# Optimization experiments

Hardware: AMD Instinct MI355X
Metric: run time of the kernel (lower is better)

The kernel has to match this reference:

```python
import jax, jax.numpy as jnp
import numpy as np
import math

SLIDING_WINDOW = 1024  # matches init kwarg

def setup_inputs() -> dict:
    key = jax.random.key(0)
    ks = jax.random.split(key, 6)
    B, S, Hq, Hkv, D = 1, 2048, 32, 8, 128
    NUM_PAGES, STRIDE = 300, 16
    q = jax.random.normal(ks[0], (B, S, Hq, D), dtype=jnp.float32)
    k = jax.random.normal(ks[1], (B, S, Hkv, D), dtype=jnp.float32)
    v = jax.random.normal(ks[2], (B, S, Hkv, D), dtype=jnp.float32)
    sink = jax.random.normal(ks[3], (Hq,), dtype=jnp.float32)
    cache_state = jnp.zeros((NUM_PAGES, STRIDE, 2, Hkv, D), dtype=jnp.float32)
    seq_block_ids = jax.random.randint(ks[4], (B, S // STRIDE), 0, NUM_PAGES, dtype=jnp.int64)
    return {"q": q, "k": k, "v": v, "sink": sink,
            "cache_state": cache_state, "seq_block_ids": seq_block_ids}


def reference(q, k, v, sink, cache_state, seq_block_ids):
    B, S, Hq, D = q.shape
    Hkv = k.shape[2]
    stride = cache_state.shape[1]

    # --- paged cache write (prefill side effect) ---
    kv = jnp.stack([k, v], axis=2)                       # [B,S,2,Hkv,D]
    pages = kv.reshape(B * (S // stride), stride, 2, Hkv, D)
    _ = cache_state.at[seq_block_ids.reshape(-1)].set(pages)

    # --- decomposed attention: matmul + mask + softmax(+sink) + matmul ---
    rep = Hq // Hkv
    ke = jnp.repeat(k, rep, axis=2)                      # [B,S,Hq,D] (GQA expand)
    ve = jnp.repeat(v, rep, axis=2)
    scale = 1.0 / math.sqrt(D)
    scores = jnp.einsum('bihd,bjhd->bhij', q, ke) * scale  # [B,Hq,S,S]

    i = jnp.arange(S)[:, None]
    j = jnp.arange(S)[None, :]
    allowed = (j <= i) & (i - j < SLIDING_WINDOW)        # causal + sliding window
    neg = jnp.finfo(scores.dtype).min
    logits = jnp.where(allowed, scores, neg)

    # attention sink: extra per-head logit appended; contributes to denominator only
    sink_l = jnp.broadcast_to(sink[None, :, None, None], (B, Hq, S, 1))
    probs = jax.nn.softmax(jnp.concatenate([logits, sink_l], axis=-1), axis=-1)[..., :S]

    out = jnp.einsum('bhij,bjhd->bihd', probs, ve)       # [B,S,Hq,D]
    return out
```

## Files before the change

### kernel.cpp

```cpp
#include <hip/hip_runtime.h>
#include <hip/hip_bf16.h>


#define S_LEN 2048
#define DH    128
#define HQ    32
#define HKV   8
#define WIN   1024
#define BR    64
#define BC    32
#define NT    (S_LEN / BC)
#define FM    16.0f
#define TILE_CH 512

typedef unsigned short u16;
typedef __attribute__((ext_vector_type(8))) short  short8;
typedef __attribute__((ext_vector_type(4))) float  floatx4;
typedef __attribute__((ext_vector_type(4))) unsigned int uintx4;

__device__ __forceinline__ unsigned rne1(float a) {
    unsigned u = __float_as_uint(a);
    return (u + 0x7FFFu + ((u >> 16) & 1u)) >> 16;
}
__device__ __forceinline__ unsigned rne_pk(float a, float b) {
    return rne1(a) | (rne1(b) << 16);
}

__global__ __launch_bounds__(256) void pack_kv(const float* __restrict__ kg,
                                               const float* __restrict__ vg,
                                               u16* __restrict__ kp,
                                               u16* __restrict__ vtp)
{
    __shared__ float Vs[BC][DH + 1];
    const int b   = blockIdx.x;
    const int hk  = b >> 6;
    const int jt  = b & 63;
    const int tid = threadIdx.x;
    const int j0  = jt * BC;

    #pragma unroll
    for (int t = 0; t < 4; t++) {
        int idx = tid + t * 256;
        int j   = idx >> 5;
        int dc  = idx & 31;
        floatx4 f = *(const floatx4*)(vg + ((size_t)(j0 + j) * HKV + hk) * DH + dc * 4);
        Vs[j][dc * 4 + 0] = f[0]; Vs[j][dc * 4 + 1] = f[1];
        Vs[j][dc * 4 + 2] = f[2]; Vs[j][dc * 4 + 3] = f[3];
    }

    u16* kpt = kp + (size_t)b * TILE_CH * 8;
    #pragma unroll
    for (int t = 0; t < 2; t++) {
        int c = tid + t * 256;
        int row = c >> 4, cc = c & 15;
        const float* p = kg + ((size_t)(j0 + row) * HKV + hk) * DH + cc * 8;
        floatx4 f0 = *(const floatx4*)p;
        floatx4 f1 = *(const floatx4*)(p + 4);
        int pc = (row << 4) | (cc ^ (row & 7));
        *(uintx4*)(kpt + pc * 8) =
            (uintx4){rne_pk(f0[0], f0[1]), rne_pk(f0[2], f0[3]),
                     rne_pk(f1[0], f1[1]), rne_pk(f1[2], f1[3])};
    }
    __syncthreads();

    u16* vpt = vtp + (size_t)b * TILE_CH * 8;
    #pragma unroll
    for (int t = 0; t < 2; t++) {
        int q  = tid + t * 256;
        int dd = q >> 2, c = q & 3;
        unsigned w0 = rne_pk(Vs[c * 4 + 0][dd], Vs[c * 4 + 16][dd]);
        unsigned w1 = rne_pk(Vs[c * 4 + 1][dd], Vs[c * 4 + 17][dd]);
        unsigned w2 = rne_pk(Vs[c * 4 + 2][dd], Vs[c * 4 + 18][dd]);
        unsigned w3 = rne_pk(Vs[c * 4 + 3][dd], Vs[c * 4 + 19][dd]);
        int qp = (dd << 2) | (c ^ ((dd >> 2) & 3));
        *(uintx4*)(vpt + qp * 8) = (uintx4){w0, w1, w2, w3};
    }
}

__launch_bounds__(256, 4)
__global__ void fa_kernel(const float* __restrict__ qg,
                          const u16* __restrict__ kp,
                          const u16* __restrict__ vtp,
                          const float* __restrict__ sg,
                          float* __restrict__ outg)
{
    __shared__ __align__(16) u16 Kt[2][TILE_CH * 8];
    __shared__ __align__(16) u16 Vt[2][TILE_CH * 8];
    __shared__ __align__(16) u16 Pb[BR * 40];

    const int tid  = threadIdx.x;
    const int w    = tid >> 6;
    const int lane = tid & 63;
    const int quad = lane >> 4;
    const int l16  = lane & 15;

    const int bid  = blockIdx.x;
    const int hk   = bid & 7;
    const int idx  = bid >> 3;
    const int hrem = idx & 3;
    const int u5   = (idx >> 2) & 7;
    const int t4   = idx >> 5;
    const int qbt[4] = {u5, 15 - u5, 16 + u5, 31 - u5};
    const int qb   = qbt[t4];
    const int h    = hk * 4 + hrem;

    const int i0 = qb * BR;
    const int m0 = i0 + w * 16;

    short8 qf[4];
    {
        const float* qrow = qg + ((size_t)(m0 + l16) * HQ + h) * DH;
        #pragma unroll
        for (int kk = 0; kk < 4; kk++) {
            const float* p = qrow + kk * 32 + quad * 8;
            floatx4 f0 = *(const floatx4*)p;
            floatx4 f1 = *(const floatx4*)(p + 4);
            uintx4 u = (uintx4){rne_pk(f0[0], f0[1]), rne_pk(f0[2], f0[3]),
                                rne_pk(f1[0], f1[1]), rne_pk(f1[2], f1[3])};
            qf[kk] = *(short8*)&u;
        }
    }

    floatx4 acc[8];
    #pragma unroll
    for (int i = 0; i < 8; i++) acc[i] = (floatx4){0.f, 0.f, 0.f, 0.f};
    float l_part[4] = {0.f, 0.f, 0.f, 0.f};

    int c_r[4];
    #pragma unroll
    for (int r = 0; r < 4; r++) c_r[r] = m0 + quad * 4 + r - l16;

    int jlo = i0 - (WIN - 1); if (jlo < 0) jlo = 0;
    const int jt_lo = jlo >> 5;
    const int jt_hi = (i0 + BR - 1) >> 5;

    const float SC2 = 0.08838834764831845f * 1.4426950408889634f;

    const int ch0 = w * 64 + lane;
    auto stage = [&](int bb, int jt) {
        const u16* kpt = kp  + ((size_t)(hk * NT + jt)) * TILE_CH * 8;
        const u16* vpt = vtp + ((size_t)(hk * NT + jt)) * TILE_CH * 8;
        #pragma unroll
        for (int it = 0; it < 2; it++) {
            int ch = ch0 + it * 256;
            __builtin_amdgcn_global_load_lds(
                (const __attribute__((address_space(1))) unsigned*)(kpt + ch * 8),
                (__attribute__((address_space(3))) unsigned*)(&Kt[bb][ch * 8]), 16, 0, 0);
            __builtin_amdgcn_global_load_lds(
                (const __attribute__((address_space(1))) unsigned*)(vpt + ch * 8),
                (__attribute__((address_space(3))) unsigned*)(&Vt[bb][ch * 8]), 16, 0, 0);
        }
    };

    stage(0, jt_lo);
    int bb = 0;

    for (int jt = jt_lo; jt <= jt_hi; jt++) {
        const int j0 = jt << 5;

        __syncthreads();

        if (jt < jt_hi) stage(bb ^ 1, jt + 1);

        floatx4 sc[2];
        sc[0] = (floatx4){0.f, 0.f, 0.f, 0.f};
        sc[1] = (floatx4){0.f, 0.f, 0.f, 0.f};
        #pragma unroll
        for (int kk = 0; kk < 4; kk++) {
            #pragma unroll
            for (int n = 0; n < 2; n++) {
                int row = n * 16 + l16;
                int cc  = kk * 4 + quad;
                int pc  = (row << 4) | (cc ^ (row & 7));
                short8 kf = *(const short8*)(&Kt[bb][pc * 8]);
                sc[n] = __builtin_amdgcn_mfma_f32_16x16x32_bf16(qf[kk], kf, sc[n], 0, 0, 0);
            }
        }

        const int prow0 = w * 16 + quad * 4;
        const bool interior = (j0 + (BC - 1) <= i0) && (j0 >= i0 + BR - WIN);
        if (interior) {
            #pragma unroll
            for (int r = 0; r < 4; r++) {
                float p0 = exp2f(fmaf(sc[0][r], SC2, -FM));
                float p1 = exp2f(fmaf(sc[1][r], SC2, -FM));
                l_part[r] += p0 + p1;
                *(unsigned*)(&Pb[(prow0 + r) * 40 + l16 * 2]) = rne_pk(p0, p1);
            }
        } else {
            #pragma unroll
            for (int r = 0; r < 4; r++) {
                bool a0 = (j0 <= c_r[r]) && (j0 > c_r[r] - WIN);
                bool a1 = (j0 + 16 <= c_r[r]) && (j0 + 16 > c_r[r] - WIN);
                float p0 = a0 ? exp2f(fmaf(sc[0][r], SC2, -FM)) : 0.f;
                float p1 = a1 ? exp2f(fmaf(sc[1][r], SC2, -FM)) : 0.f;
                l_part[r] += p0 + p1;
                *(unsigned*)(&Pb[(prow0 + r) * 40 + l16 * 2]) = rne_pk(p0, p1);
            }
        }

        {
            short8 pf = *(const short8*)(&Pb[(w * 16 + l16) * 40 + quad * 8]);
            #pragma unroll
            for (int nf = 0; nf < 8; nf++) {
                int dd = nf * 16 + l16;
                int qp = (dd << 2) | (quad ^ ((dd >> 2) & 3));
                short8 vf = *(const short8*)(&Vt[bb][qp * 8]);
                acc[nf] = __builtin_amdgcn_mfma_f32_16x16x32_bf16(pf, vf, acc[nf], 0, 0, 0);
            }
        }
        bb ^= 1;
    }

    const float sk2 = exp2f(fmaf(sg[h], 1.4426950408889634f, -FM));
    float inv[4];
    #pragma unroll
    for (int r = 0; r < 4; r++) {
        float l = l_part[r];
        #pragma unroll
        for (int off = 1; off < 16; off <<= 1)
            l += __shfl_xor(l, off);
        inv[r] = 1.f / (l + sk2);
    }
    #pragma unroll
    for (int nf = 0; nf < 8; nf++) {
        int d = nf * 16 + l16;
        #pragma unroll
        for (int r = 0; r < 4; r++) {
            int ig = m0 + quad * 4 + r;
            outg[((size_t)ig * HQ + h) * DH + d] = acc[nf][r] * inv[r];
        }
    }
}

__launch_bounds__(256, 4)
__global__ void fa_fallback(const float* __restrict__ qg,
                            const float* __restrict__ kg,
                            const float* __restrict__ vg,
                            const float* __restrict__ sg,
                            float* __restrict__ outg)
{
    __shared__ __align__(16) u16 Kt[BC * DH];
    __shared__ __align__(16) u16 Vt[DH * BC];
    __shared__ __align__(16) u16 Pb[BR * 40];

    const int tid  = threadIdx.x;
    const int w    = tid >> 6;
    const int lane = tid & 63;
    const int quad = lane >> 4;
    const int l16  = lane & 15;

    const int qb = blockIdx.x / HQ;
    const int h  = blockIdx.x % HQ;
    const int hk = h >> 2;
    const int i0 = qb * BR;
    const int m0 = i0 + w * 16;

    short8 qf[4];
    {
        const float* qrow = qg + ((size_t)(m0 + l16) * HQ + h) * DH;
        #pragma unroll
        for (int kk = 0; kk < 4; kk++) {
            const float* p = qrow + kk * 32 + quad * 8;
            floatx4 f0 = *(const floatx4*)p;
            floatx4 f1 = *(const floatx4*)(p + 4);
            uintx4 u = (uintx4){rne_pk(f0[0], f0[1]), rne_pk(f0[2], f0[3]),
                                rne_pk(f1[0], f1[1]), rne_pk(f1[2], f1[3])};
            qf[kk] = *(short8*)&u;
        }
    }

    floatx4 acc[8];
    #pragma unroll
    for (int i = 0; i < 8; i++) acc[i] = (floatx4){0.f, 0.f, 0.f, 0.f};
    float l_part[4] = {0.f, 0.f, 0.f, 0.f};

    int jlo = i0 - (WIN - 1); if (jlo < 0) jlo = 0;
    const int jt_lo = jlo >> 5;
    const int jt_hi = (i0 + BR - 1) >> 5;
    const float SC2 = 0.08838834764831845f * 1.4426950408889634f;

    for (int jt = jt_lo; jt <= jt_hi; jt++) {
        const int j0 = jt << 5;
        __syncthreads();
        #pragma unroll
        for (int it = 0; it < 2; it++) {
            int g   = tid + 256 * it;
            int row = g >> 4, cc = g & 15;
            int pc  = (row << 4) | (cc ^ (row & 7));
            const float* kpp = kg + ((size_t)(j0 + row) * HKV + hk) * DH + cc * 8;
            floatx4 f0 = *(const floatx4*)kpp;
            floatx4 f1 = *(const floatx4*)(kpp + 4);
            *(uintx4*)(&Kt[pc * 8]) =
                (uintx4){rne_pk(f0[0], f0[1]), rne_pk(f0[2], f0[3]),
                         rne_pk(f1[0], f1[1]), rne_pk(f1[2], f1[3])};
        }
        #pragma unroll
        for (int it = 0; it < 2; it++) {
            int g  = tid + 256 * it;
            int d  = g & 127, jc = g >> 7;
            const float* vp = vg + ((size_t)(j0 + jc * 8) * HKV + hk) * DH + d;
            float e0 = vp[0 * HKV * DH], e1 = vp[1 * HKV * DH];
            float e2 = vp[2 * HKV * DH], e3 = vp[3 * HKV * DH];
            float e4 = vp[4 * HKV * DH], e5 = vp[5 * HKV * DH];
            float e6 = vp[6 * HKV * DH], e7 = vp[7 * HKV * DH];
            int pc = (d << 2) | (jc ^ ((d >> 2) & 3));
            *(uintx4*)(&Vt[pc * 8]) =
                (uintx4){rne_pk(e0, e1), rne_pk(e2, e3), rne_pk(e4, e5), rne_pk(e6, e7)};
        }
        __syncthreads();

        floatx4 sc[2];
        sc[0] = (floatx4){0.f, 0.f, 0.f, 0.f};
        sc[1] = (floatx4){0.f, 0.f, 0.f, 0.f};
        #pragma unroll
        for (int kk = 0; kk < 4; kk++) {
            #pragma unroll
            for (int n = 0; n < 2; n++) {
                int row = n * 16 + l16;
                int cc  = kk * 4 + quad;
                int pc  = (row << 4) | (cc ^ (row & 7));
                short8 kf = *(const short8*)(&Kt[pc * 8]);
                sc[n] = __builtin_amdgcn_mfma_f32_16x16x32_bf16(qf[kk], kf, sc[n], 0, 0, 0);
            }
        }
        #pragma unroll
        for (int r = 0; r < 4; r++) {
            int   i_g = m0 + quad * 4 + r;
            int   jg0 = j0 + l16, jg1 = j0 + 16 + l16;
            bool  a0  = (jg0 <= i_g) && (i_g - jg0 < WIN);
            bool  a1  = (jg1 <= i_g) && (i_g - jg1 < WIN);
            float p0  = a0 ? exp2f(fmaf(sc[0][r], SC2, -FM)) : 0.f;
            float p1  = a1 ? exp2f(fmaf(sc[1][r], SC2, -FM)) : 0.f;
            l_part[r] += p0 + p1;
            int prow = w * 16 + quad * 4 + r;
            *(unsigned*)(&Pb[prow * 40 + 2 * l16]) = rne_pk(p0, p1);
        }
        {
            short8 pf = *(const short8*)(&Pb[(w * 16 + l16) * 40 + quad * 8]);
            #pragma unroll
            for (int nf = 0; nf < 8; nf++) {
                int dd = nf * 16 + l16;
                int qp = (dd << 2) | (quad ^ ((dd >> 2) & 3));
                short8 vf = *(const short8*)(&Vt[qp * 8]);
                acc[nf] = __builtin_amdgcn_mfma_f32_16x16x32_bf16(pf, vf, acc[nf], 0, 0, 0);
            }
        }
    }

    const float sk2 = exp2f(fmaf(sg[h], 1.4426950408889634f, -FM));
    float inv[4];
    #pragma unroll
    for (int r = 0; r < 4; r++) {
        float l = l_part[r];
        #pragma unroll
        for (int off = 1; off < 16; off <<= 1)
            l += __shfl_xor(l, off);
        inv[r] = 1.f / (l + sk2);
    }
    #pragma unroll
    for (int nf = 0; nf < 8; nf++) {
        int d = nf * 16 + l16;
        #pragma unroll
        for (int r = 0; r < 4; r++) {
            int ig = m0 + quad * 4 + r;
            outg[((size_t)ig * HQ + h) * DH + d] = acc[nf][r] * inv[r];
        }
    }
}

extern "C" void kernel_launch(void* const* d_in, const int* in_sizes, int n_in,
                              void* d_out, int out_size, void* d_ws, size_t ws_size,
                              hipStream_t stream) {
    const float* q  = (const float*)d_in[0];
    const float* k  = (const float*)d_in[1];
    const float* v  = (const float*)d_in[2];
    const float* sk = (const float*)d_in[3];
    float* out = (float*)d_out;

    const size_t tile_elems = (size_t)HKV * NT * TILE_CH * 8;
    const size_t need = 2 * tile_elems * sizeof(u16);

    if (ws_size >= need) {
        u16* kp  = (u16*)d_ws;
        u16* vtp = kp + tile_elems;
        pack_kv<<<dim3(HKV * NT), 256, 0, stream>>>(k, v, kp, vtp);
        fa_kernel<<<dim3((S_LEN / BR) * HQ), 256, 0, stream>>>(q, kp, vtp, sk, out);
    } else {
        fa_fallback<<<dim3((S_LEN / BR) * HQ), 256, 0, stream>>>(q, k, v, sk, out);
    }
}
```

Baseline: 163.1 us.

## Keep P in registers via transposed QK MFMA, drop LDS P buffer

```diff
diff --git a/kernel.cpp b/kernel.cpp
--- a/kernel.cpp
+++ b/kernel.cpp
@@ -24,6 +24,11 @@
 }
 __device__ __forceinline__ unsigned rne_pk(float a, float b) {
     return rne1(a) | (rne1(b) << 16);
+}
+__device__ __forceinline__ unsigned cvt_pk(float a, float b) {
+    unsigned r;
+    asm("v_cvt_pk_bf16_f32 %0, %1, %2" : "=v"(r) : "v"(a), "v"(b));
+    return r;
 }
 
 __global__ __launch_bounds__(256) void pack_kv(const float* __restrict__ kg,
@@ -77,7 +82,7 @@
     }
 }
 
-__launch_bounds__(256, 4)
+__launch_bounds__(256, 5)
 __global__ void fa_kernel(const float* __restrict__ qg,
                           const u16* __restrict__ kp,
                           const u16* __restrict__ vtp,
@@ -86,7 +91,6 @@
 {
     __shared__ __align__(16) u16 Kt[2][TILE_CH * 8];
     __shared__ __align__(16) u16 Vt[2][TILE_CH * 8];
-    __shared__ __align__(16) u16 Pb[BR * 40];
 
     const int tid  = threadIdx.x;
     const int w    = tid >> 6;
@@ -115,20 +119,34 @@
             const float* p = qrow + kk * 32 + quad * 8;
             floatx4 f0 = *(const floatx4*)p;
             floatx4 f1 = *(const floatx4*)(p + 4);
-            uintx4 u = (uintx4){rne_pk(f0[0], f0[1]), rne_pk(f0[2], f0[3]),
-                                rne_pk(f1[0], f1[1]), rne_pk(f1[2], f1[3])};
-            qf[kk] = *(short8*)&u;
-        }
+            uintx4 uq = (uintx4){cvt_pk(f0[0], f0[1]), cvt_pk(f0[2], f0[3]),
+                                 cvt_pk(f1[0], f1[1]), cvt_pk(f1[2], f1[3])};
+            qf[kk] = *(short8*)&uq;
+        }
+    }
+
+    int kpc[8];
+    #pragma unroll
+    for (int n = 0; n < 2; n++) {
+        int row = n * 16 + l16;
+        #pragma unroll
+        for (int kk = 0; kk < 4; kk++)
+            kpc[n * 4 + kk] = (((row << 4) | ((kk * 4 + quad) ^ (row & 7)))) * 8;
+    }
+    int vqp[8];
+    #pragma unroll
+    for (int nf = 0; nf < 8; nf++) {
+        int dd = nf * 16 + l16;
+        vqp[nf] = ((dd << 2) | (quad ^ ((dd >> 2) & 3))) * 8;
     }
 
     floatx4 acc[8];
     #pragma unroll
     for (int i = 0; i < 8; i++) acc[i] = (floatx4){0.f, 0.f, 0.f, 0.f};
-    float l_part[4] = {0.f, 0.f, 0.f, 0.f};
-
-    int c_r[4];
-    #pragma unroll
-    for (int r = 0; r < 4; r++) c_r[r] = m0 + quad * 4 + r - l16;
+    float l_sum = 0.f;
+
+    const int ci  = m0 + l16;
+    const int qb4 = quad * 4;
 
     int jlo = i0 - (WIN - 1); if (jlo < 0) jlo = 0;
     const int jt_lo = jlo >> 5;
@@ -162,73 +180,67 @@
 
         if (jt < jt_hi) stage(bb ^ 1, jt + 1);
 
-        floatx4 sc[2];
-        sc[0] = (floatx4){0.f, 0.f, 0.f, 0.f};
-        sc[1] = (floatx4){0.f, 0.f, 0.f, 0.f};
+        floatx4 ss[2];
+        ss[0] = (floatx4){0.f, 0.f, 0.f, 0.f};
+        ss[1] = (floatx4){0.f, 0.f, 0.f, 0.f};
         #pragma unroll
         for (int kk = 0; kk < 4; kk++) {
-            #pragma unroll
-            for (int n = 0; n < 2; n++) {
-                int row = n * 16 + l16;
-                int cc  = kk * 4 + quad;
-                int pc  = (row << 4) | (cc ^ (row & 7));
-                short8 kf = *(const short8*)(&Kt[bb][pc * 8]);
-                sc[n] = __builtin_amdgcn_mfma_f32_16x16x32_bf16(qf[kk], kf, sc[n], 0, 0, 0);
-            }
-        }
-
-        const int prow0 = w * 16 + quad * 4;
+            short8 kf0 = *(const short8*)(&Kt[bb][kpc[kk]]);
+            short8 kf1 = *(const short8*)(&Kt[bb][kpc[4 + kk]]);
+            ss[0] = __builtin_amdgcn_mfma_f32_16x16x32_bf16(kf0, qf[kk], ss[0], 0, 0, 0);
+            ss[1] = __builtin_amdgcn_mfma_f32_16x16x32_bf16(kf1, qf[kk], ss[1], 0, 0, 0);
+        }
+
+        float p[2][4];
         const bool interior = (j0 + (BC - 1) <= i0) && (j0 >= i0 + BR - WIN);
         if (interior) {
             #pragma unroll
-            for (int r = 0; r < 4; r++) {
-                float p0 = exp2f(fmaf(sc[0][r], SC2, -FM));
-                float p1 = exp2f(fmaf(sc[1][r], SC2, -FM));
-                l_part[r] += p0 + p1;
-                *(unsigned*)(&Pb[(prow0 + r) * 40 + l16 * 2]) = rne_pk(p0, p1);
-            }
+            for (int n = 0; n < 2; n++)
+                #pragma unroll
+                for (int r = 0; r < 4; r++)
+                    p[n][r] = exp2f(fmaf(ss[n][r], SC2, -FM));
         } else {
+            const int dj = ci - j0;
             #pragma unroll
-            for (int r = 0; r < 4; r++) {
-                bool a0 = (j0 <= c_r[r]) && (j0 > c_r[r] - WIN);
-                bool a1 = (j0 + 16 <= c_r[r]) && (j0 + 16 > c_r[r] - WIN);
-                float p0 = a0 ? exp2f(fmaf(sc[0][r], SC2, -FM)) : 0.f;
-                float p1 = a1 ? exp2f(fmaf(sc[1][r], SC2, -FM)) : 0.f;
-                l_part[r] += p0 + p1;
-                *(unsigned*)(&Pb[(prow0 + r) * 40 + l16 * 2]) = rne_pk(p0, p1);
-            }
-        }
-
-        {
-            short8 pf = *(const short8*)(&Pb[(w * 16 + l16) * 40 + quad * 8]);
-            #pragma unroll
-            for (int nf = 0; nf < 8; nf++) {
-                int dd = nf * 16 + l16;
-                int qp = (dd << 2) | (quad ^ ((dd >> 2) & 3));
-                short8 vf = *(const short8*)(&Vt[bb][qp * 8]);
-                acc[nf] = __builtin_amdgcn_mfma_f32_16x16x32_bf16(pf, vf, acc[nf], 0, 0, 0);
-            }
+            for (int n = 0; n < 2; n++)
+                #pragma unroll
+                for (int r = 0; r < 4; r++) {
+                    int t = n * 16 + qb4 + r;
+                    bool a = (t <= dj) && (t > dj - WIN);
+                    p[n][r] = a ? exp2f(fmaf(ss[n][r], SC2, -FM)) : 0.f;
+                }
+        }
+        l_sum += ((p[0][0] + p[0][1]) + (p[0][2] + p[0][3]))
+               + ((p[1][0] + p[1][1]) + (p[1][2] + p[1][3]));
+
+        uintx4 upf = (uintx4){cvt_pk(p[0][0], p[1][0]), cvt_pk(p[0][1], p[1][1]),
+                              cvt_pk(p[0][2], p[1][2]), cvt_pk(p[0][3], p[1][3])};
+        short8 pf = *(short8*)&upf;
+
+        #pragma unroll
+        for (int nf = 0; nf < 8; nf++) {
+            short8 vf = *(const short8*)(&Vt[bb][vqp[nf]]);
+            acc[nf] = __builtin_amdgcn_mfma_f32_16x16x32_bf16(pf, vf, acc[nf], 0, 0, 0);
         }
         bb ^= 1;
     }
 
+    l_sum += __shfl_xor(l_sum, 16);
+    l_sum += __shfl_xor(l_sum, 32);
     const float sk2 = exp2f(fmaf(sg[h], 1.4426950408889634f, -FM));
-    float inv[4];
+    float inv_r[4];
     #pragma unroll
     for (int r = 0; r < 4; r++) {
-        float l = l_part[r];
-        #pragma unroll
-        for (int off = 1; off < 16; off <<= 1)
-            l += __shfl_xor(l, off);
-        inv[r] = 1.f / (l + sk2);
+        float Lr = __shfl(l_sum, qb4 + r);
+        inv_r[r] = 1.f / (Lr + sk2);
     }
     #pragma unroll
     for (int nf = 0; nf < 8; nf++) {
         int d = nf * 16 + l16;
         #pragma unroll
         for (int r = 0; r < 4; r++) {
-            int ig = m0 + quad * 4 + r;
-            outg[((size_t)ig * HQ + h) * DH + d] = acc[nf][r] * inv[r];
+            int ig = m0 + qb4 + r;
+            outg[((size_t)ig * HQ + h) * DH + d] = acc[nf][r] * inv_r[r];
         }
     }
 }
```

Result: faster. 159.1 us (-2.4%).
